# Kernel tuning notes

Measured on AMD Instinct MI355X. Metric: run time of the kernel, lower is better.

## Reference

```python
import jax, jax.numpy as jnp
import numpy as np

SR = 16000
HOP = 256
MIN_F0 = 50.0
MAX_F0 = 500.0
MIN_PERIOD = SR // 500          # 32
MAX_PERIOD = SR // 50           # 320
FRAME_LEN = HOP * 2             # 512
LAG_END = min(MAX_PERIOD, FRAME_LEN // 2)  # 256 -> lags 32..255 (224 lags)


def setup_inputs() -> dict:
    key = jax.random.key(0)
    waveform = jax.random.normal(key, (64, 1, 163840), dtype=jnp.float32)
    return {"waveform": waveform}


def reference(waveform):
    B, C, T = waveform.shape
    x = waveform[:, 0, :]  # (B, T)
    pad = FRAME_LEN // 2
    xpad = jnp.pad(x, ((0, 0), (pad, pad)), mode='reflect')
    n_frames = (T + 2 * pad - FRAME_LEN) // HOP + 1  # = T//HOP + 1
    # frame extraction (equivalent to unfold(frame_length, hop))
    idx = np.arange(n_frames)[:, None] * HOP + np.arange(FRAME_LEN)[None, :]
    frames = xpad[:, idx]  # (B, F, L)
    # L2-normalize each frame
    norm = jnp.sqrt(jnp.sum(frames * frames, axis=-1, keepdims=True))
    xn = frames / (norm + 1e-8)
    # zero-pad right so xn[t] * xz[t+p] reproduces frame[:L-p] * frame[p:]
    xz = jnp.pad(xn, ((0, 0), (0, 0), (0, FRAME_LEN)))
    lags = jnp.arange(MIN_PERIOD, LAG_END)

    def step(carry, p):
        sl = jax.lax.dynamic_slice_in_dim(xz, p, FRAME_LEN, axis=-1)
        return carry, jnp.sum(xn * sl, axis=-1)  # (B, F)

    _, ac = jax.lax.scan(step, None, lags)  # (P, B, F)
    max_idx = jnp.argmax(ac, axis=0)  # (B, F)
    period = max_idx.astype(jnp.float32) + MIN_PERIOD
    f0 = SR / (period + 1e-8)
    return jnp.clip(f0, MIN_F0, MAX_F0)  # (B, F)
```

## Files before the change

kernel.cpp:

```cpp
#include <hip/hip_runtime.h>


#define SR_F 16000.0f
#define HOP 256
#define FRAME_LEN 512
#define PAD 256
#define T_LEN 163840
#define N_FRAMES 641
#define MIN_PERIOD 32
#define N_LAGS 224
#define FPB 8

typedef _Float16 half8 __attribute__((ext_vector_type(8)));
typedef float floatx4 __attribute__((ext_vector_type(4)));

__device__ __forceinline__ int swz(int q) { return q ^ ((q >> 3) & 7); }

__device__ __forceinline__ unsigned int pkh(float a, float b) {
    unsigned short ha = __builtin_bit_cast(unsigned short, (_Float16)a);
    unsigned short hb = __builtin_bit_cast(unsigned short, (_Float16)b);
    return (unsigned int)ha | ((unsigned int)hb << 16);
}

__device__ __forceinline__ void write_copies(unsigned int* e, unsigned int* o,
                                             unsigned int u10, unsigned int u11,
                                             unsigned int u20, unsigned int u21,
                                             int lane) {
    e[120 + 2*lane] = u10;  e[121 + 2*lane] = u11;
    e[248 + 2*lane] = u20;  e[249 + 2*lane] = u21;
    unsigned int a  = __shfl(u10, (lane + 1) & 63);
    unsigned int bb = __shfl(u20, (lane + 1) & 63);
    unsigned int n1 = (lane == 63) ? bb : a;
    unsigned int n2 = (lane == 63) ? 0u : bb;
    o[120 + 2*lane] = (u10 >> 16) | (u11 << 16);
    o[121 + 2*lane] = (u11 >> 16) | (n1 << 16);
    o[248 + 2*lane] = (u20 >> 16) | (u21 << 16);
    o[249 + 2*lane] = (u21 >> 16) | (n2 << 16);
    if (lane == 0) o[119] = u10 << 16;
}

__global__ __launch_bounds__(512, 4) void f0_kernel(const float* __restrict__ wav,
                                                    float* __restrict__ out) {
    __shared__ unsigned int yw[FPB][1600];

    const int tid  = threadIdx.x;
    const int wv   = tid >> 6;
    const int lane = tid & 63;
    const int bf   = blockIdx.x * FPB + wv;
    const int b    = bf / N_FRAMES;
    const int f    = bf - b * N_FRAMES;
    const float* __restrict__ x = wav + (size_t)b * T_LEN;
    unsigned int* ye  = yw[wv];
    unsigned int* yo  = ye + 400;
    unsigned int* le  = ye + 800;
    unsigned int* loo = ye + 1200;
    const int base = f * HOP - PAD;
    const bool fast = (f != 0 && f != N_FRAMES - 1);

    ye[lane] = 0u; yo[lane] = 0u;
    if (lane < 56) { ye[64 + lane] = 0u; yo[64 + lane] = 0u; }
    if (lane < 25) { ye[375 + lane] = 0u; yo[375 + lane] = 0u; }

    float qen = 0.0f;
    if (fast) {
        const float4* g4 = (const float4*)(x + base);
        float4 c1 = g4[lane];
        float4 c2 = g4[lane + 64];
        qen = c1.x*c1.x + c1.y*c1.y + c1.z*c1.z + c1.w*c1.w
            + c2.x*c2.x + c2.y*c2.y + c2.z*c2.z + c2.w*c2.w;
        write_copies(ye, yo, pkh(c1.x, c1.y), pkh(c1.z, c1.w),
                             pkh(c2.x, c2.y), pkh(c2.z, c2.w), lane);
    } else {
        for (int t = lane; t < FRAME_LEN; t += 64) {
            int idx = base + t;
            if (idx < 0) idx = -idx;
            if (idx >= T_LEN) idx = 2 * (T_LEN - 1) - idx;
            float v = x[idx];
            qen = __builtin_fmaf(v, v, qen);
            unsigned short h = __builtin_bit_cast(unsigned short, (_Float16)v);
            ((unsigned short*)ye)[240 + t] = h;
            ((unsigned short*)yo)[239 + t] = h;
        }
    }
    __threadfence_block();

    #pragma unroll
    for (int m = 1; m < 64; m <<= 1) qen += __shfl_xor(qen, m);

    const int qd = lane >> 4;
    const int nn = lane & 15;
    const int par = nn & 1;
    const unsigned int* ybh = par ? yo : ye;
    const int wA0 = 120 + 4*qd - 8*nn;
    const int wB0 = 136 + 4*qd + ((nn - par) >> 1);

    floatx4 acc = {0.f, 0.f, 0.f, 0.f};
    #pragma unroll
    for (int c = 0; c < 16; ++c) {
        uint4 au = *(const uint4*)(ye + (wA0 + 16*c));
        const unsigned int* pb = ybh + (wB0 + 16*c);
        uint4 bu; bu.x = pb[0]; bu.y = pb[1]; bu.z = pb[2]; bu.w = pb[3];
        acc = __builtin_amdgcn_mfma_f32_16x16x32_f16(
            __builtin_bit_cast(half8, au), __builtin_bit_cast(half8, bu),
            acc, 0, 0, 0);
    }

    float v1 = acc[0];
    int   i1 = 64*qd + nn;
    float v2 = -__builtin_inff();
    #pragma unroll
    for (int r = 1; r < 4; ++r) {
        float cv = (4*qd + r < 14) ? acc[r] : -__builtin_inff();
        bool take = (cv > v1);
        float lose = take ? v1 : cv;
        if (take) { v1 = cv; i1 = 64*qd + 16*r + nn; }
        v2 = fmaxf(v2, lose);
    }
    #pragma unroll
    for (int m = 1; m < 64; m <<= 1) {
        float ov1 = __shfl_xor(v1, m);
        float ov2 = __shfl_xor(v2, m);
        int   oi1 = __shfl_xor(i1, m);
        bool take = (ov1 > v1) || (ov1 == v1 && oi1 < i1);
        float lose = take ? v1 : ov1;
        if (take) { v1 = ov1; i1 = oi1; }
        v2 = fmaxf(fmaxf(v2, ov2), lose);
    }

    const float E1 = 9.765625e-4f * qen + 0.05f;
    if (v1 - v2 > 2.0f * E1) {
        if (lane == 0) {
            float period = (float)(i1 + MIN_PERIOD);
            float f0 = SR_F / (period + 1e-8f);
            out[bf] = fminf(fmaxf(f0, 50.0f), 500.0f);
        }
        return;
    }

    le[lane] = 0u; loo[lane] = 0u;
    if (lane < 56) { le[64 + lane] = 0u; loo[64 + lane] = 0u; }
    if (lane < 25) { le[375 + lane] = 0u; loo[375 + lane] = 0u; }
    if (fast) {
        const float4* g4 = (const float4*)(x + base);
        float4 c1 = g4[lane];
        float4 c2 = g4[lane + 64];
        float l0 = c1.x - (float)(_Float16)c1.x;
        float l1 = c1.y - (float)(_Float16)c1.y;
        float l2 = c1.z - (float)(_Float16)c1.z;
        float l3 = c1.w - (float)(_Float16)c1.w;
        float l4 = c2.x - (float)(_Float16)c2.x;
        float l5 = c2.y - (float)(_Float16)c2.y;
        float l6 = c2.z - (float)(_Float16)c2.z;
        float l7 = c2.w - (float)(_Float16)c2.w;
        write_copies(le, loo, pkh(l0, l1), pkh(l2, l3),
                              pkh(l4, l5), pkh(l6, l7), lane);
    } else {
        for (int t = lane; t < FRAME_LEN; t += 64) {
            int idx = base + t;
            if (idx < 0) idx = -idx;
            if (idx >= T_LEN) idx = 2 * (T_LEN - 1) - idx;
            float v = x[idx];
            float l = v - (float)(_Float16)v;
            unsigned short h = __builtin_bit_cast(unsigned short, (_Float16)l);
            ((unsigned short*)le)[240 + t] = h;
            ((unsigned short*)loo)[239 + t] = h;
        }
    }
    __threadfence_block();

    const unsigned int* ybl = par ? loo : le;
    #pragma unroll
    for (int c = 0; c < 16; ++c) {
        uint4 au = *(const uint4*)(ye + (wA0 + 16*c));
        const unsigned int* pb = ybl + (wB0 + 16*c);
        uint4 bu; bu.x = pb[0]; bu.y = pb[1]; bu.z = pb[2]; bu.w = pb[3];
        acc = __builtin_amdgcn_mfma_f32_16x16x32_f16(
            __builtin_bit_cast(half8, au), __builtin_bit_cast(half8, bu),
            acc, 0, 0, 0);
    }
    #pragma unroll
    for (int c = 0; c < 16; ++c) {
        uint4 au = *(const uint4*)(le + (wA0 + 16*c));
        const unsigned int* pb = ybh + (wB0 + 16*c);
        uint4 bu; bu.x = pb[0]; bu.y = pb[1]; bu.z = pb[2]; bu.w = pb[3];
        acc = __builtin_amdgcn_mfma_f32_16x16x32_f16(
            __builtin_bit_cast(half8, au), __builtin_bit_cast(half8, bu),
            acc, 0, 0, 0);
    }

    v1 = acc[0]; i1 = 64*qd + nn; v2 = -__builtin_inff();
    #pragma unroll
    for (int r = 1; r < 4; ++r) {
        float cv = (4*qd + r < 14) ? acc[r] : -__builtin_inff();
        bool take = (cv > v1);
        float lose = take ? v1 : cv;
        if (take) { v1 = cv; i1 = 64*qd + 16*r + nn; }
        v2 = fmaxf(v2, lose);
    }
    #pragma unroll
    for (int m = 1; m < 64; m <<= 1) {
        float ov1 = __shfl_xor(v1, m);
        float ov2 = __shfl_xor(v2, m);
        int   oi1 = __shfl_xor(i1, m);
        bool take = (ov1 > v1) || (ov1 == v1 && oi1 < i1);
        float lose = take ? v1 : ov1;
        if (take) { v1 = ov1; i1 = oi1; }
        v2 = fmaxf(fmaxf(v2, ov2), lose);
    }

    const float E2 = 1.0e-4f * qen + 0.02f;
    if (v1 - v2 > 2.0f * E2) {
        if (lane == 0) {
            float period = (float)(i1 + MIN_PERIOD);
            float f0 = SR_F / (period + 1e-8f);
            out[bf] = fminf(fmaxf(f0, 50.0f), 500.0f);
        }
        return;
    }

    float* sw = (float*)ye;
    if (fast) {
        const float4* g4 = (const float4*)(x + base);
        ((float4*)sw)[swz(lane)]      = g4[lane];
        ((float4*)sw)[swz(lane + 64)] = g4[lane + 64];
        if (lane < 16) ((float4*)sw)[swz(lane + 128)] = make_float4(0.f,0.f,0.f,0.f);
    } else {
        for (int t = lane; t < FRAME_LEN; t += 64) {
            int idx = base + t;
            if (idx < 0) idx = -idx;
            if (idx >= T_LEN) idx = 2 * (T_LEN - 1) - idx;
            sw[(swz(t >> 2) << 2) | (t & 3)] = x[idx];
        }
        int t = FRAME_LEN + lane;
        sw[(swz(t >> 2) << 2) | (t & 3)] = 0.0f;
    }
    __threadfence_block();

    const float4* s4 = (const float4*)sw;
    const int seg = lane & 15;
    const bool s0 = (seg & 1), s1 = (seg & 2), s2 = (seg & 4), s3 = (seg & 8);

    double dtot[4];
    #pragma unroll
    for (int r = 0; r < 4; ++r) {
        const int g  = (r << 2) + qd;
        const int p0 = MIN_PERIOD + (g << 4);
        double dacc[16];
        #pragma unroll
        for (int j = 0; j < 16; ++j) dacc[j] = 0.0;
        if (g < 14) {
            const int n16 = (FRAME_LEN - p0 + 15) >> 4;
            #pragma unroll
            for (int k = 0; k < 2; ++k) {
                const int ch = seg + (k << 4);
                if (ch < n16) {
                    const int t  = ch << 4;
                    const int qa = t >> 2;
                    const int qw = (t + p0) >> 2;
                    float a[16], w[32];
                    #pragma unroll
                    for (int u = 0; u < 4; ++u) {
                        float4 v = s4[swz(qa + u)];
                        a[4*u+0]=v.x; a[4*u+1]=v.y; a[4*u+2]=v.z; a[4*u+3]=v.w;
                    }
                    #pragma unroll
                    for (int u = 0; u < 8; ++u) {
                        float4 v = s4[swz(qw + u)];
                        w[4*u+0]=v.x; w[4*u+1]=v.y; w[4*u+2]=v.z; w[4*u+3]=v.w;
                    }
                    #pragma unroll
                    for (int j = 0; j < 16; ++j) {
                        #pragma unroll
                        for (int i = 0; i < 16; ++i)
                            dacc[j] = fma((double)a[i], (double)w[i + j], dacc[j]);
                    }
                }
            }
        }
        double u8[8], u4[4], u2[2], dtotal;
        #pragma unroll
        for (int i = 0; i < 8; ++i) {
            double lo = dacc[2*i], hi = dacc[2*i+1];
            double keep = s0 ? hi : lo, send = s0 ? lo : hi;
            u8[i] = keep + __shfl_xor(send, 1);
        }
        #pragma unroll
        for (int i = 0; i < 4; ++i) {
            double lo = u8[2*i], hi = u8[2*i+1];
            double keep = s1 ? hi : lo, send = s1 ? lo : hi;
            u4[i] = keep + __shfl_xor(send, 2);
        }
        #pragma unroll
        for (int i = 0; i < 2; ++i) {
            double lo = u4[2*i], hi = u4[2*i+1];
            double keep = s2 ? hi : lo, send = s2 ? lo : hi;
            u2[i] = keep + __shfl_xor(send, 4);
        }
        {
            double lo = u2[0], hi = u2[1];
            double keep = s3 ? hi : lo, send = s3 ? lo : hi;
            dtotal = keep + __shfl_xor(send, 8);
        }
        dtot[r] = ((r << 6) + lane < N_LAGS) ? dtotal : -__builtin_inf();
    }
    double dv1 = dtot[0];
    int    di1 = lane;
    #pragma unroll
    for (int r = 1; r < 4; ++r) {
        double c = dtot[r];
        if (c > dv1) { dv1 = c; di1 = (r << 6) + lane; }
    }
    #pragma unroll
    for (int m = 1; m < 64; m <<= 1) {
        double o = __shfl_xor(dv1, m);
        int   oi = __shfl_xor(di1, m);
        if (o > dv1 || (o == dv1 && oi < di1)) { dv1 = o; di1 = oi; }
    }
    if (lane == 0) {
        float period = (float)(di1 + MIN_PERIOD);
        float f0 = SR_F / (period + 1e-8f);
        out[bf] = fminf(fmaxf(f0, 50.0f), 500.0f);
    }
}

extern "C" void kernel_launch(void* const* d_in, const int* in_sizes, int n_in,
                              void* d_out, int out_size, void* d_ws, size_t ws_size,
                              hipStream_t stream) {
    const float* wav = (const float*)d_in[0];
    float* out = (float*)d_out;
    const int n_blocks = (64 * N_FRAMES) / FPB;
    f0_kernel<<<n_blocks, 512, 0, stream>>>(wav, out);
}
```

Baseline: 141.2 us.

## Process several frames per wavefront in a loop with smaller blocks

Each wavefront now loops over 8 consecutive frames instead of handling one, with 4 waves per 256-thread block, so there are far fewer blocks. The first MFMA pass splits into two independent accumulators to shorten the dependency chain, and the frame's global loads are kept in registers for the residual pass instead of being reloaded. This cuts per-block launch overhead and lets early-exit frames hand their time to the next frame, at the cost of less parallelism and possible load imbalance across waves. GAP_B32 is defined but unused.

```diff
diff --git a/kernel.cpp b/kernel.cpp
--- a/kernel.cpp
+++ b/kernel.cpp
@@ -9,7 +9,9 @@
 #define N_FRAMES 641
 #define MIN_PERIOD 32
 #define N_LAGS 224
-#define FPB 8
+#define WPB 4
+#define FPW 8
+#define GAP_B32 0.0625f
 
 typedef _Float16 half8 __attribute__((ext_vector_type(8)));
 typedef float floatx4 __attribute__((ext_vector_type(4)));
@@ -39,287 +41,299 @@
     if (lane == 0) o[119] = u10 << 16;
 }
 
-__global__ __launch_bounds__(512, 4) void f0_kernel(const float* __restrict__ wav,
+__global__ __launch_bounds__(256, 4) void f0_kernel(const float* __restrict__ wav,
                                                     float* __restrict__ out) {
-    __shared__ unsigned int yw[FPB][1600];
+    __shared__ unsigned int yw[WPB][1600];
 
     const int tid  = threadIdx.x;
     const int wv   = tid >> 6;
     const int lane = tid & 63;
-    const int bf   = blockIdx.x * FPB + wv;
-    const int b    = bf / N_FRAMES;
-    const int f    = bf - b * N_FRAMES;
-    const float* __restrict__ x = wav + (size_t)b * T_LEN;
     unsigned int* ye  = yw[wv];
     unsigned int* yo  = ye + 400;
     unsigned int* le  = ye + 800;
     unsigned int* loo = ye + 1200;
-    const int base = f * HOP - PAD;
-    const bool fast = (f != 0 && f != N_FRAMES - 1);
-
-    ye[lane] = 0u; yo[lane] = 0u;
-    if (lane < 56) { ye[64 + lane] = 0u; yo[64 + lane] = 0u; }
-    if (lane < 25) { ye[375 + lane] = 0u; yo[375 + lane] = 0u; }
-
-    float qen = 0.0f;
-    if (fast) {
-        const float4* g4 = (const float4*)(x + base);
-        float4 c1 = g4[lane];
-        float4 c2 = g4[lane + 64];
-        qen = c1.x*c1.x + c1.y*c1.y + c1.z*c1.z + c1.w*c1.w
-            + c2.x*c2.x + c2.y*c2.y + c2.z*c2.z + c2.w*c2.w;
-        write_copies(ye, yo, pkh(c1.x, c1.y), pkh(c1.z, c1.w),
-                             pkh(c2.x, c2.y), pkh(c2.z, c2.w), lane);
-    } else {
-        for (int t = lane; t < FRAME_LEN; t += 64) {
-            int idx = base + t;
-            if (idx < 0) idx = -idx;
-            if (idx >= T_LEN) idx = 2 * (T_LEN - 1) - idx;
-            float v = x[idx];
-            qen = __builtin_fmaf(v, v, qen);
-            unsigned short h = __builtin_bit_cast(unsigned short, (_Float16)v);
-            ((unsigned short*)ye)[240 + t] = h;
-            ((unsigned short*)yo)[239 + t] = h;
-        }
-    }
-    __threadfence_block();
-
-    #pragma unroll
-    for (int m = 1; m < 64; m <<= 1) qen += __shfl_xor(qen, m);
 
     const int qd = lane >> 4;
     const int nn = lane & 15;
     const int par = nn & 1;
     const unsigned int* ybh = par ? yo : ye;
+    const unsigned int* ybl = par ? loo : le;
     const int wA0 = 120 + 4*qd - 8*nn;
     const int wB0 = 136 + 4*qd + ((nn - par) >> 1);
-
-    floatx4 acc = {0.f, 0.f, 0.f, 0.f};
-    #pragma unroll
-    for (int c = 0; c < 16; ++c) {
-        uint4 au = *(const uint4*)(ye + (wA0 + 16*c));
-        const unsigned int* pb = ybh + (wB0 + 16*c);
-        uint4 bu; bu.x = pb[0]; bu.y = pb[1]; bu.z = pb[2]; bu.w = pb[3];
-        acc = __builtin_amdgcn_mfma_f32_16x16x32_f16(
-            __builtin_bit_cast(half8, au), __builtin_bit_cast(half8, bu),
-            acc, 0, 0, 0);
-    }
-
-    float v1 = acc[0];
-    int   i1 = 64*qd + nn;
-    float v2 = -__builtin_inff();
-    #pragma unroll
-    for (int r = 1; r < 4; ++r) {
-        float cv = (4*qd + r < 14) ? acc[r] : -__builtin_inff();
-        bool take = (cv > v1);
-        float lose = take ? v1 : cv;
-        if (take) { v1 = cv; i1 = 64*qd + 16*r + nn; }
-        v2 = fmaxf(v2, lose);
-    }
-    #pragma unroll
-    for (int m = 1; m < 64; m <<= 1) {
-        float ov1 = __shfl_xor(v1, m);
-        float ov2 = __shfl_xor(v2, m);
-        int   oi1 = __shfl_xor(i1, m);
-        bool take = (ov1 > v1) || (ov1 == v1 && oi1 < i1);
-        float lose = take ? v1 : ov1;
-        if (take) { v1 = ov1; i1 = oi1; }
-        v2 = fmaxf(fmaxf(v2, ov2), lose);
-    }
-
-    const float E1 = 9.765625e-4f * qen + 0.05f;
-    if (v1 - v2 > 2.0f * E1) {
+    const int seg = lane & 15;
+    const bool s0 = (seg & 1), s1 = (seg & 2), s2 = (seg & 4), s3 = (seg & 8);
+
+    const int bf0 = (blockIdx.x * WPB + wv) * FPW;
+
+    for (int it = 0; it < FPW; ++it) {
+        const int bf = bf0 + it;
+        const int b  = bf / N_FRAMES;
+        const int f  = bf - b * N_FRAMES;
+        const float* __restrict__ x = wav + (size_t)b * T_LEN;
+        const int base = f * HOP - PAD;
+        const bool fast = (f != 0 && f != N_FRAMES - 1);
+
+        float4 c1, c2;
+        if (fast) {
+            const float4* g4 = (const float4*)(x + base);
+            c1 = g4[lane];
+            c2 = g4[lane + 64];
+        }
+        ye[lane] = 0u; yo[lane] = 0u;
+        if (lane < 56) { ye[64 + lane] = 0u; yo[64 + lane] = 0u; }
+        if (lane < 25) { ye[375 + lane] = 0u; yo[375 + lane] = 0u; }
+
+        float qen = 0.0f;
+        if (fast) {
+            qen = c1.x*c1.x + c1.y*c1.y + c1.z*c1.z + c1.w*c1.w
+                + c2.x*c2.x + c2.y*c2.y + c2.z*c2.z + c2.w*c2.w;
+            write_copies(ye, yo, pkh(c1.x, c1.y), pkh(c1.z, c1.w),
+                                 pkh(c2.x, c2.y), pkh(c2.z, c2.w), lane);
+        } else {
+            for (int t = lane; t < FRAME_LEN; t += 64) {
+                int idx = base + t;
+                if (idx < 0) idx = -idx;
+                if (idx >= T_LEN) idx = 2 * (T_LEN - 1) - idx;
+                float v = x[idx];
+                qen = __builtin_fmaf(v, v, qen);
+                unsigned short h = __builtin_bit_cast(unsigned short, (_Float16)v);
+                ((unsigned short*)ye)[240 + t] = h;
+                ((unsigned short*)yo)[239 + t] = h;
+            }
+        }
+        __threadfence_block();
+
+        #pragma unroll
+        for (int m = 1; m < 64; m <<= 1) qen += __shfl_xor(qen, m);
+
+        floatx4 acc0 = {0.f, 0.f, 0.f, 0.f};
+        floatx4 acc1 = {0.f, 0.f, 0.f, 0.f};
+        #pragma unroll
+        for (int c = 0; c < 16; c += 2) {
+            uint4 au0 = *(const uint4*)(ye + (wA0 + 16*c));
+            const unsigned int* pb0 = ybh + (wB0 + 16*c);
+            uint4 bu0; bu0.x=pb0[0]; bu0.y=pb0[1]; bu0.z=pb0[2]; bu0.w=pb0[3];
+            uint4 au1 = *(const uint4*)(ye + (wA0 + 16*(c+1)));
+            const unsigned int* pb1 = ybh + (wB0 + 16*(c+1));
+            uint4 bu1; bu1.x=pb1[0]; bu1.y=pb1[1]; bu1.z=pb1[2]; bu1.w=pb1[3];
+            acc0 = __builtin_amdgcn_mfma_f32_16x16x32_f16(
+                __builtin_bit_cast(half8, au0), __builtin_bit_cast(half8, bu0),
+                acc0, 0, 0, 0);
+            acc1 = __builtin_amdgcn_mfma_f32_16x16x32_f16(
+                __builtin_bit_cast(half8, au1), __builtin_bit_cast(half8, bu1),
+                acc1, 0, 0, 0);
+        }
+        floatx4 acc = acc0 + acc1;
+
+        float v1 = acc[0];
+        int   i1 = 64*qd + nn;
+        float v2 = -__builtin_inff();
+        #pragma unroll
+        for (int r = 1; r < 4; ++r) {
+            float cv = (4*qd + r < 14) ? acc[r] : -__builtin_inff();
+            bool take = (cv > v1);
+            float lose = take ? v1 : cv;
+            if (take) { v1 = cv; i1 = 64*qd + 16*r + nn; }
+            v2 = fmaxf(v2, lose);
+        }
+        #pragma unroll
+        for (int m = 1; m < 64; m <<= 1) {
+            float ov1 = __shfl_xor(v1, m);
+            float ov2 = __shfl_xor(v2, m);
+            int   oi1 = __shfl_xor(i1, m);
+            bool take = (ov1 > v1) || (ov1 == v1 && oi1 < i1);
+            float lose = take ? v1 : ov1;
+            if (take) { v1 = ov1; i1 = oi1; }
+            v2 = fmaxf(fmaxf(v2, ov2), lose);
+        }
+
+        const float E1 = 9.765625e-4f * qen + 0.05f;
+        if (v1 - v2 > 2.0f * E1) {
+            if (lane == 0) {
+                float period = (float)(i1 + MIN_PERIOD);
+                float f0 = SR_F / (period + 1e-8f);
+                out[bf] = fminf(fmaxf(f0, 50.0f), 500.0f);
+            }
+            continue;
+        }
+
+        le[lane] = 0u; loo[lane] = 0u;
+        if (lane < 56) { le[64 + lane] = 0u; loo[64 + lane] = 0u; }
+        if (lane < 25) { le[375 + lane] = 0u; loo[375 + lane] = 0u; }
+        if (fast) {
+            float l0 = c1.x - (float)(_Float16)c1.x;
+            float l1 = c1.y - (float)(_Float16)c1.y;
+            float l2 = c1.z - (float)(_Float16)c1.z;
+            float l3 = c1.w - (float)(_Float16)c1.w;
+            float l4 = c2.x - (float)(_Float16)c2.x;
+            float l5 = c2.y - (float)(_Float16)c2.y;
+            float l6 = c2.z - (float)(_Float16)c2.z;
+            float l7 = c2.w - (float)(_Float16)c2.w;
+            write_copies(le, loo, pkh(l0, l1), pkh(l2, l3),
+                                  pkh(l4, l5), pkh(l6, l7), lane);
+        } else {
+            for (int t = lane; t < FRAME_LEN; t += 64) {
+                int idx = base + t;
+                if (idx < 0) idx = -idx;
+                if (idx >= T_LEN) idx = 2 * (T_LEN - 1) - idx;
+                float v = x[idx];
+                float l = v - (float)(_Float16)v;
+                unsigned short h = __builtin_bit_cast(unsigned short, (_Float16)l);
+                ((unsigned short*)le)[240 + t] = h;
+                ((unsigned short*)loo)[239 + t] = h;
+            }
+        }
+        __threadfence_block();
+
+        #pragma unroll
+        for (int c = 0; c < 16; ++c) {
+            uint4 au = *(const uint4*)(ye + (wA0 + 16*c));
+            const unsigned int* pb = ybl + (wB0 + 16*c);
+            uint4 bu; bu.x = pb[0]; bu.y = pb[1]; bu.z = pb[2]; bu.w = pb[3];
+            acc = __builtin_amdgcn_mfma_f32_16x16x32_f16(
+                __builtin_bit_cast(half8, au), __builtin_bit_cast(half8, bu),
+                acc, 0, 0, 0);
+        }
+        #pragma unroll
+        for (int c = 0; c < 16; ++c) {
+            uint4 au = *(const uint4*)(le + (wA0 + 16*c));
+            const unsigned int* pb = ybh + (wB0 + 16*c);
+            uint4 bu; bu.x = pb[0]; bu.y = pb[1]; bu.z = pb[2]; bu.w = pb[3];
+            acc = __builtin_amdgcn_mfma_f32_16x16x32_f16(
+                __builtin_bit_cast(half8, au), __builtin_bit_cast(half8, bu),
+                acc, 0, 0, 0);
+        }
+
+        v1 = acc[0]; i1 = 64*qd + nn; v2 = -__builtin_inff();
+        #pragma unroll
+        for (int r = 1; r < 4; ++r) {
+            float cv = (4*qd + r < 14) ? acc[r] : -__builtin_inff();
+            bool take = (cv > v1);
+            float lose = take ? v1 : cv;
+            if (take) { v1 = cv; i1 = 64*qd + 16*r + nn; }
+            v2 = fmaxf(v2, lose);
+        }
+        #pragma unroll
+        for (int m = 1; m < 64; m <<= 1) {
+            float ov1 = __shfl_xor(v1, m);
+            float ov2 = __shfl_xor(v2, m);
+            int   oi1 = __shfl_xor(i1, m);
+            bool take = (ov1 > v1) || (ov1 == v1 && oi1 < i1);
+            float lose = take ? v1 : ov1;
+            if (take) { v1 = ov1; i1 = oi1; }
+            v2 = fmaxf(fmaxf(v2, ov2), lose);
+        }
+
+        const float E2 = 1.0e-4f * qen + 0.02f;
+        if (v1 - v2 > 2.0f * E2) {
+            if (lane == 0) {
+                float period = (float)(i1 + MIN_PERIOD);
+                float f0 = SR_F / (period + 1e-8f);
+                out[bf] = fminf(fmaxf(f0, 50.0f), 500.0f);
+            }
+            continue;
+        }
+
+        float* sw = (float*)ye;
+        if (fast) {
+            const float4* g4 = (const float4*)(x + base);
+            ((float4*)sw)[swz(lane)]      = g4[lane];
+            ((float4*)sw)[swz(lane + 64)] = g4[lane + 64];
+            if (lane < 16) ((float4*)sw)[swz(lane + 128)] = make_float4(0.f,0.f,0.f,0.f);
+        } else {
+            for (int t = lane; t < FRAME_LEN; t += 64) {
+                int idx = base + t;
+                if (idx < 0) idx = -idx;
+                if (idx >= T_LEN) idx = 2 * (T_LEN - 1) - idx;
+                sw[(swz(t >> 2) << 2) | (t & 3)] = x[idx];
+            }
+            int t = FRAME_LEN + lane;
+            sw[(swz(t >> 2) << 2) | (t & 3)] = 0.0f;
+        }
+        __threadfence_block();
+
+        const float4* s4 = (const float4*)sw;
+        double dtot[4];
+        #pragma unroll
+        for (int r = 0; r < 4; ++r) {
+            const int g  = (r << 2) + qd;
+            const int p0 = MIN_PERIOD + (g << 4);
+            double dacc[16];
+            #pragma unroll
+            for (int j = 0; j < 16; ++j) dacc[j] = 0.0;
+            if (g < 14) {
+                const int n16 = (FRAME_LEN - p0 + 15) >> 4;
+                #pragma unroll
+                for (int k = 0; k < 2; ++k) {
+                    const int ch = seg + (k << 4);
+                    if (ch < n16) {
+                        const int t  = ch << 4;
+                        const int qa = t >> 2;
+                        const int qw = (t + p0) >> 2;
+                        float a[16], w[32];
+                        #pragma unroll
+                        for (int u = 0; u < 4; ++u) {
+                            float4 v = s4[swz(qa + u)];
+                            a[4*u+0]=v.x; a[4*u+1]=v.y; a[4*u+2]=v.z; a[4*u+3]=v.w;
+                        }
+                        #pragma unroll
+                        for (int u = 0; u < 8; ++u) {
+                            float4 v = s4[swz(qw + u)];
+                            w[4*u+0]=v.x; w[4*u+1]=v.y; w[4*u+2]=v.z; w[4*u+3]=v.w;
+                        }
+                        #pragma unroll
+                        for (int j = 0; j < 16; ++j) {
+                            #pragma unroll
+                            for (int i = 0; i < 16; ++i)
+                                dacc[j] = fma((double)a[i], (double)w[i + j], dacc[j]);
+                        }
+                    }
+                }
+            }
+            double u8[8], u4[4], u2[2], dtotal;
+            #pragma unroll
+            for (int i = 0; i < 8; ++i) {
+                double lo = dacc[2*i], hi = dacc[2*i+1];
+                double keep = s0 ? hi : lo, send = s0 ? lo : hi;
+                u8[i] = keep + __shfl_xor(send, 1);
+            }
+            #pragma unroll
+            for (int i = 0; i < 4; ++i) {
+                double lo = u8[2*i], hi = u8[2*i+1];
+                double keep = s1 ? hi : lo, send = s1 ? lo : hi;
+                u4[i] = keep + __shfl_xor(send, 2);
+            }
+            #pragma unroll
+            for (int i = 0; i < 2; ++i) {
+                double lo = u4[2*i], hi = u4[2*i+1];
+                double keep = s2 ? hi : lo, send = s2 ? lo : hi;
+                u2[i] = keep + __shfl_xor(send, 4);
+            }
+            {
+                double lo = u2[0], hi = u2[1];
+                double keep = s3 ? hi : lo, send = s3 ? lo : hi;
+                dtotal = keep + __shfl_xor(send, 8);
+            }
+            dtot[r] = ((r << 6) + lane < N_LAGS) ? dtotal : -__builtin_inf();
+        }
+        double dv1 = dtot[0];
+        int    di1 = lane;
+        #pragma unroll
+        for (int r = 1; r < 4; ++r) {
+            double c = dtot[r];
+            if (c > dv1) { dv1 = c; di1 = (r << 6) + lane; }
+        }
+        #pragma unroll
+        for (int m = 1; m < 64; m <<= 1) {
+            double o = __shfl_xor(dv1, m);
+            int   oi = __shfl_xor(di1, m);
+            if (o > dv1 || (o == dv1 && oi < di1)) { dv1 = o; di1 = oi; }
+        }
         if (lane == 0) {
-            float period = (float)(i1 + MIN_PERIOD);
+            float period = (float)(di1 + MIN_PERIOD);
             float f0 = SR_F / (period + 1e-8f);
             out[bf] = fminf(fmaxf(f0, 50.0f), 500.0f);
         }
-        return;
-    }
-
-    le[lane] = 0u; loo[lane] = 0u;
-    if (lane < 56) { le[64 + lane] = 0u; loo[64 + lane] = 0u; }
-    if (lane < 25) { le[375 + lane] = 0u; loo[375 + lane] = 0u; }
-    if (fast) {
-        const float4* g4 = (const float4*)(x + base);
-        float4 c1 = g4[lane];
-        float4 c2 = g4[lane + 64];
-        float l0 = c1.x - (float)(_Float16)c1.x;
-        float l1 = c1.y - (float)(_Float16)c1.y;
-        float l2 = c1.z - (float)(_Float16)c1.z;
-        float l3 = c1.w - (float)(_Float16)c1.w;
-        float l4 = c2.x - (float)(_Float16)c2.x;
-        float l5 = c2.y - (float)(_Float16)c2.y;
-        float l6 = c2.z - (float)(_Float16)c2.z;
-        float l7 = c2.w - (float)(_Float16)c2.w;
-        write_copies(le, loo, pkh(l0, l1), pkh(l2, l3),
-                              pkh(l4, l5), pkh(l6, l7), lane);
-    } else {
-        for (int t = lane; t < FRAME_LEN; t += 64) {
-            int idx = base + t;
-            if (idx < 0) idx = -idx;
-            if (idx >= T_LEN) idx = 2 * (T_LEN - 1) - idx;
-            float v = x[idx];
-            float l = v - (float)(_Float16)v;
-            unsigned short h = __builtin_bit_cast(unsigned short, (_Float16)l);
-            ((unsigned short*)le)[240 + t] = h;
-            ((unsigned short*)loo)[239 + t] = h;
-        }
-    }
-    __threadfence_block();
-
-    const unsigned int* ybl = par ? loo : le;
-    #pragma unroll
-    for (int c = 0; c < 16; ++c) {
-        uint4 au = *(const uint4*)(ye + (wA0 + 16*c));
-        const unsigned int* pb = ybl + (wB0 + 16*c);
-        uint4 bu; bu.x = pb[0]; bu.y = pb[1]; bu.z = pb[2]; bu.w = pb[3];
-        acc = __builtin_amdgcn_mfma_f32_16x16x32_f16(
-            __builtin_bit_cast(half8, au), __builtin_bit_cast(half8, bu),
-            acc, 0, 0, 0);
-    }
-    #pragma unroll
-    for (int c = 0; c < 16; ++c) {
-        uint4 au = *(const uint4*)(le + (wA0 + 16*c));
-        const unsigned int* pb = ybh + (wB0 + 16*c);
-        uint4 bu; bu.x = pb[0]; bu.y = pb[1]; bu.z = pb[2]; bu.w = pb[3];
-        acc = __builtin_amdgcn_mfma_f32_16x16x32_f16(
-            __builtin_bit_cast(half8, au), __builtin_bit_cast(half8, bu),
-            acc, 0, 0, 0);
-    }
-
-    v1 = acc[0]; i1 = 64*qd + nn; v2 = -__builtin_inff();
-    #pragma unroll
-    for (int r = 1; r < 4; ++r) {
-        float cv = (4*qd + r < 14) ? acc[r] : -__builtin_inff();
-        bool take = (cv > v1);
-        float lose = take ? v1 : cv;
-        if (take) { v1 = cv; i1 = 64*qd + 16*r + nn; }
-        v2 = fmaxf(v2, lose);
-    }
-    #pragma unroll
-    for (int m = 1; m < 64; m <<= 1) {
-        float ov1 = __shfl_xor(v1, m);
-        float ov2 = __shfl_xor(v2, m);
-        int   oi1 = __shfl_xor(i1, m);
-        bool take = (ov1 > v1) || (ov1 == v1 && oi1 < i1);
-        float lose = take ? v1 : ov1;
-        if (take) { v1 = ov1; i1 = oi1; }
-        v2 = fmaxf(fmaxf(v2, ov2), lose);
-    }
-
-    const float E2 = 1.0e-4f * qen + 0.02f;
-    if (v1 - v2 > 2.0f * E2) {
-        if (lane == 0) {
-            float period = (float)(i1 + MIN_PERIOD);
-            float f0 = SR_F / (period + 1e-8f);
-            out[bf] = fminf(fmaxf(f0, 50.0f), 500.0f);
-        }
-        return;
-    }
-
-    float* sw = (float*)ye;
-    if (fast) {
-        const float4* g4 = (const float4*)(x + base);
-        ((float4*)sw)[swz(lane)]      = g4[lane];
-        ((float4*)sw)[swz(lane + 64)] = g4[lane + 64];
-        if (lane < 16) ((float4*)sw)[swz(lane + 128)] = make_float4(0.f,0.f,0.f,0.f);
-    } else {
-        for (int t = lane; t < FRAME_LEN; t += 64) {
-            int idx = base + t;
-            if (idx < 0) idx = -idx;
-            if (idx >= T_LEN) idx = 2 * (T_LEN - 1) - idx;
-            sw[(swz(t >> 2) << 2) | (t & 3)] = x[idx];
-        }
-        int t = FRAME_LEN + lane;
-        sw[(swz(t >> 2) << 2) | (t & 3)] = 0.0f;
-    }
-    __threadfence_block();
-
-    const float4* s4 = (const float4*)sw;
-    const int seg = lane & 15;
-    const bool s0 = (seg & 1), s1 = (seg & 2), s2 = (seg & 4), s3 = (seg & 8);
-
-    double dtot[4];
-    #pragma unroll
-    for (int r = 0; r < 4; ++r) {
-        const int g  = (r << 2) + qd;
-        const int p0 = MIN_PERIOD + (g << 4);
-        double dacc[16];
-        #pragma unroll
-        for (int j = 0; j < 16; ++j) dacc[j] = 0.0;
-        if (g < 14) {
-            const int n16 = (FRAME_LEN - p0 + 15) >> 4;
-            #pragma unroll
-            for (int k = 0; k < 2; ++k) {
-                const int ch = seg + (k << 4);
-                if (ch < n16) {
-                    const int t  = ch << 4;
-                    const int qa = t >> 2;
-                    const int qw = (t + p0) >> 2;
-                    float a[16], w[32];
-                    #pragma unroll
-                    for (int u = 0; u < 4; ++u) {
-                        float4 v = s4[swz(qa + u)];
-                        a[4*u+0]=v.x; a[4*u+1]=v.y; a[4*u+2]=v.z; a[4*u+3]=v.w;
-                    }
-                    #pragma unroll
-                    for (int u = 0; u < 8; ++u) {
-                        float4 v = s4[swz(qw + u)];
-                        w[4*u+0]=v.x; w[4*u+1]=v.y; w[4*u+2]=v.z; w[4*u+3]=v.w;
-                    }
-                    #pragma unroll
-                    for (int j = 0; j < 16; ++j) {
-                        #pragma unroll
-                        for (int i = 0; i < 16; ++i)
-                            dacc[j] = fma((double)a[i], (double)w[i + j], dacc[j]);
-                    }
-                }
-            }
-        }
-        double u8[8], u4[4], u2[2], dtotal;
-        #pragma unroll
-        for (int i = 0; i < 8; ++i) {
-            double lo = dacc[2*i], hi = dacc[2*i+1];
-            double keep = s0 ? hi : lo, send = s0 ? lo : hi;
-            u8[i] = keep + __shfl_xor(send, 1);
-        }
-        #pragma unroll
-        for (int i = 0; i < 4; ++i) {
-            double lo = u8[2*i], hi = u8[2*i+1];
-            double keep = s1 ? hi : lo, send = s1 ? lo : hi;
-            u4[i] = keep + __shfl_xor(send, 2);
-        }
-        #pragma unroll
-        for (int i = 0; i < 2; ++i) {
-            double lo = u4[2*i], hi = u4[2*i+1];
-            double keep = s2 ? hi : lo, send = s2 ? lo : hi;
-            u2[i] = keep + __shfl_xor(send, 4);
-        }
-        {
-            double lo = u2[0], hi = u2[1];
-            double keep = s3 ? hi : lo, send = s3 ? lo : hi;
-            dtotal = keep + __shfl_xor(send, 8);
-        }
-        dtot[r] = ((r << 6) + lane < N_LAGS) ? dtotal : -__builtin_inf();
-    }
-    double dv1 = dtot[0];
-    int    di1 = lane;
-    #pragma unroll
-    for (int r = 1; r < 4; ++r) {
-        double c = dtot[r];
-        if (c > dv1) { dv1 = c; di1 = (r << 6) + lane; }
-    }
-    #pragma unroll
-    for (int m = 1; m < 64; m <<= 1) {
-        double o = __shfl_xor(dv1, m);
-        int   oi = __shfl_xor(di1, m);
-        if (o > dv1 || (o == dv1 && oi < di1)) { dv1 = o; di1 = oi; }
-    }
-    if (lane == 0) {
-        float period = (float)(di1 + MIN_PERIOD);
-        float f0 = SR_F / (period + 1e-8f);
-        out[bf] = fminf(fmaxf(f0, 50.0f), 500.0f);
     }
 }
 
@@ -328,6 +342,6 @@
                               hipStream_t stream) {
     const float* wav = (const float*)d_in[0];
     float* out = (float*)d_out;
-    const int n_blocks = (64 * N_FRAMES) / FPB;
-    f0_kernel<<<n_blocks, 512, 0, stream>>>(wav, out);
+    const int n_blocks = (64 * N_FRAMES) / (WPB * FPW);
+    f0_kernel<<<n_blocks, 256, 0, stream>>>(wav, out);
 }
```

New measurement: 223.8 us. 1.58x slower.
